# Kernel tuning notes

Measured on AMD Instinct MI355X. Metric: run time of the kernel, lower is better.

Reference implementation:

```python
import jax, jax.numpy as jnp
import numpy as np
from jax.scipy.special import gammaln

D_MODEL = 256
N_HEADS = 8
BIAS_HIDDEN = 64
B, N = 2, 1024
EPS = 1e-4


def setup_inputs() -> dict:
    key = jax.random.key(0)
    ks = jax.random.split(key, 12)
    d, h = D_MODEL, BIAS_HIDDEN
    s = 0.02
    return {
        "src": jax.random.normal(ks[0], (B, N, d), jnp.float32),
        "coords": jax.random.normal(ks[1], (B, N, 4), jnp.float32),
        "Wq": jax.random.normal(ks[2], (d, d), jnp.float32) * s,
        "Wk": jax.random.normal(ks[3], (d, d), jnp.float32) * s,
        "Wv": jax.random.normal(ks[4], (d, d), jnp.float32) * s,
        "Wo": jax.random.normal(ks[5], (d, d), jnp.float32) * s,
        "gw1": jax.random.normal(ks[6], (h, 2), jnp.float32) * s,
        "gb1": jnp.zeros((h,), jnp.float32),
        "gw2": jax.random.normal(ks[7], (1, h), jnp.float32) * s,
        "gb2": jnp.zeros((1,), jnp.float32),
        "dw1": jax.random.normal(ks[8], (h, 4), jnp.float32) * s,
        "db1": jnp.zeros((h,), jnp.float32),
        "dw2": jax.random.normal(ks[9], (2, h), jnp.float32) * s,
        "db2": jnp.zeros((2,), jnp.float32),
    }


def reference(src, coords, Wq, Wk, Wv, Wo, gw1, gb1, gw2, gb2, dw1, db1, dw2, db2):
    Bb, Nn, d = src.shape
    H = N_HEADS
    dh = d // H
    scale = 1.0 / np.sqrt(dh).astype(np.float32)

    def split_heads(x):  # [B,N,d] -> [B,H,N,dh]
        return x.reshape(Bb, Nn, H, dh).transpose(0, 2, 1, 3)

    q = split_heads(src @ Wq.T)
    k = split_heads(src @ Wk.T)
    v = split_heads(src @ Wv.T)

    attn = jnp.einsum("bhnd,bhmd->bhnm", q, k) * scale  # [B,H,N,N]

    xyz = coords[..., :3]
    t = coords[..., 3]
    delta = xyz[:, :, None, :] - xyz[:, None, :, :]        # [B,N,N,3]
    dist = jnp.linalg.norm(delta, axis=-1)                  # [B,N,N]
    dt = t[:, :, None] - t[:, None, :]                      # [B,N,N]

    # geometric bias MLP: 2 -> hidden -> 1
    geom_feat = jnp.stack((dist, dt), axis=-1)              # [B,N,N,2]
    gh = jax.nn.relu(geom_feat @ gw1.T + gb1)
    bias = (gh @ gw2.T + gb2)[..., 0]                       # [B,N,N]

    # delay bias MLP: [dist, xyz_j] (4) -> hidden -> 2 (Gamma shape, rate)
    xyz_j = jnp.broadcast_to(xyz[:, None, :, :], (Bb, Nn, Nn, 3))
    delay_feat = jnp.concatenate((dist[..., None], xyz_j), axis=-1)  # [B,N,N,4]
    dhid = jax.nn.relu(delay_feat @ dw1.T + db1)
    raw = dhid @ dw2.T + db2                                # [B,N,N,2]
    shape = jax.nn.softplus(raw[..., 0]) + EPS
    rate = jax.nn.softplus(raw[..., 1]) + EPS
    dt_pos = jnp.maximum(jnp.abs(dt), EPS)
    # Gamma(shape, rate).log_prob(x)
    log_prob = (shape * jnp.log(rate) + (shape - 1.0) * jnp.log(dt_pos)
                - rate * dt_pos - gammaln(shape))
    bias = bias + log_prob

    attn = attn + bias[:, None, :, :]
    weights = jax.nn.softmax(attn, axis=-1)
    out = jnp.einsum("bhnm,bhmd->bhnd", weights, v)
    out = out.transpose(0, 2, 1, 3).reshape(Bb, Nn, d)
    return out @ Wo.T
```

## Files before the change

kernel.cpp:

```cpp
#include <hip/hip_runtime.h>
#include <hip/hip_bf16.h>
#include <math.h>

constexpr int B_ = 2;
constexpr int N_ = 1024;
constexpr int D_ = 256;
constexpr int H_ = 8;
constexpr int DH_ = 32;
constexpr float SCALE_ = 0.17677669529663687f;
constexpr float LOG2E_ = 1.4426950408889634f;
constexpr float SCALE2_ = SCALE_ * LOG2E_;
constexpr float EPSV_ = 1e-4f;

typedef __attribute__((ext_vector_type(8))) short short8;
typedef __attribute__((ext_vector_type(4))) float f32x4;

__device__ __forceinline__ unsigned short f2bf(float x) {
  __hip_bfloat16 h = __float2bfloat16(x);
  return __builtin_bit_cast(unsigned short, h);
}
__device__ __forceinline__ float bf2f(unsigned short u) {
  unsigned int x = ((unsigned int)u) << 16;
  return __builtin_bit_cast(float, x);
}

__device__ __forceinline__ void split8(const float* __restrict__ p,
                                       short8& hi, short8& lo) {
  f32x4 f0 = *(const f32x4*)p;
  f32x4 f1 = *(const f32x4*)(p + 4);
#pragma unroll
  for (int i = 0; i < 4; ++i) {
    unsigned short h0 = f2bf(f0[i]);
    hi[i] = (short)h0;
    lo[i] = (short)f2bf(f0[i] - bf2f(h0));
    unsigned short h1 = f2bf(f1[i]);
    hi[4 + i] = (short)h1;
    lo[4 + i] = (short)f2bf(f1[i] - bf2f(h1));
  }
}

__device__ __forceinline__ float lgamma_fast(float x) {
  float y = (x < 1.f) ? x : (x - 1.f);
  float g = fmaf(y, 0.035868343f, -0.193527818f);
  g = fmaf(y, g, 0.482199394f);
  g = fmaf(y, g, -0.756704078f);
  g = fmaf(y, g, 0.918206857f);
  g = fmaf(y, g, -0.897056937f);
  g = fmaf(y, g, 0.988205891f);
  g = fmaf(y, g, -0.577191652f);
  g = fmaf(y, g, 1.0f);
  float lg = __logf(g);
  return (x < 1.f) ? lg - __logf(x) : lg;
}
__device__ __forceinline__ float softplus_fast(float x) {
  return __logf(1.f + __expf(x));
}

__device__ __forceinline__
void mfma_proj_wave_f32(const float* __restrict__ A, const float* __restrict__ W,
                        int r0, int c0, f32x4 (&acc)[4]) {
  const int l = threadIdx.x & 63;
  const int lr = l & 15, lg = l >> 4;
#pragma unroll
  for (int ct = 0; ct < 4; ++ct) acc[ct] = (f32x4){0.f, 0.f, 0.f, 0.f};
#pragma unroll 2
  for (int ks = 0; ks < 8; ++ks) {
    short8 ahi, alo;
    split8(A + (size_t)(r0 + lr) * D_ + ks * 32 + lg * 8, ahi, alo);
#pragma unroll
    for (int ct = 0; ct < 4; ++ct) {
      short8 wh, wl;
      split8(W + (size_t)(c0 + ct * 16 + lr) * D_ + ks * 32 + lg * 8, wh, wl);
      acc[ct] = __builtin_amdgcn_mfma_f32_16x16x32_bf16(ahi, wh, acc[ct], 0, 0, 0);
      acc[ct] = __builtin_amdgcn_mfma_f32_16x16x32_bf16(alo, wh, acc[ct], 0, 0, 0);
      acc[ct] = __builtin_amdgcn_mfma_f32_16x16x32_bf16(ahi, wl, acc[ct], 0, 0, 0);
    }
  }
}

__device__ __forceinline__
void mfma_wave_pure(const unsigned short* __restrict__ Ahi,
                    const unsigned short* __restrict__ Alo,
                    const unsigned short* __restrict__ whi,
                    const unsigned short* __restrict__ wlo,
                    int r0, int c0, f32x4 (&acc)[4]) {
  const int l = threadIdx.x & 63;
  const int lr = l & 15, lg = l >> 4;
#pragma unroll
  for (int ct = 0; ct < 4; ++ct) acc[ct] = (f32x4){0.f, 0.f, 0.f, 0.f};
#pragma unroll 2
  for (int ks = 0; ks < 8; ++ks) {
    size_t aoff = (size_t)(r0 + lr) * D_ + ks * 32 + lg * 8;
    short8 ahi = *(const short8*)(Ahi + aoff);
    short8 alo = *(const short8*)(Alo + aoff);
#pragma unroll
    for (int ct = 0; ct < 4; ++ct) {
      size_t woff = (size_t)(c0 + ct * 16 + lr) * D_ + ks * 32 + lg * 8;
      short8 wh = *(const short8*)(whi + woff);
      short8 wl = *(const short8*)(wlo + woff);
      acc[ct] = __builtin_amdgcn_mfma_f32_16x16x32_bf16(ahi, wh, acc[ct], 0, 0, 0);
      acc[ct] = __builtin_amdgcn_mfma_f32_16x16x32_bf16(alo, wh, acc[ct], 0, 0, 0);
      acc[ct] = __builtin_amdgcn_mfma_f32_16x16x32_bf16(ahi, wl, acc[ct], 0, 0, 0);
    }
  }
}

__global__ __launch_bounds__(256)
void fused1_kernel(const float* __restrict__ coords,
                   const float* __restrict__ gw1, const float* __restrict__ gb1,
                   const float* __restrict__ gw2, const float* __restrict__ gb2,
                   const float* __restrict__ dw1, const float* __restrict__ db1,
                   const float* __restrict__ dw2, const float* __restrict__ db2,
                   float* __restrict__ bias,
                   const float* __restrict__ Wq, const float* __restrict__ Wk,
                   const float* __restrict__ Wv, const float* __restrict__ Wo,
                   const float* __restrict__ src,
                   unsigned short* __restrict__ whi, unsigned short* __restrict__ wlo,
                   unsigned short* __restrict__ qbf, unsigned short* __restrict__ kbf,
                   unsigned short* __restrict__ vtbf) {
  const int tid = threadIdx.x;
  const int bi = blockIdx.x;

  if (bi >= 2432) {
    int idx = ((bi - 2432) * 256 + tid) * 4;
    float4 f = *(const float4*)(Wo + idx);
    ushort4 hi, lo;
    hi.x = f2bf(f.x); lo.x = f2bf(f.x - bf2f(hi.x));
    hi.y = f2bf(f.y); lo.y = f2bf(f.y - bf2f(hi.y));
    hi.z = f2bf(f.z); lo.z = f2bf(f.z - bf2f(hi.z));
    hi.w = f2bf(f.w); lo.w = f2bf(f.w - bf2f(hi.w));
    *(ushort4*)(whi + 3 * 65536 + idx) = hi;
    *(ushort4*)(wlo + 3 * 65536 + idx) = lo;
    return;
  }

  if (bi >= 2048) {
    const int bi2 = bi - 2048;
    const int z = bi2 >> 7;
    const float* W = (z == 0) ? Wq : (z == 1) ? Wk : Wv;
    const int rem = bi2 & 127;
    const int by = rem >> 5, bx = rem & 31;
    const int w = tid >> 6;
    const int r0 = bx * 64 + w * 16;
    const int c0 = by * 64;
    f32x4 acc[4];
    mfma_proj_wave_f32(src, W, r0, c0, acc);

    const int l = tid & 63, lr = l & 15, lg = l >> 4;
    if (z < 2) {
      unsigned short* dst = (z == 0) ? qbf : kbf;
#pragma unroll
      for (int ct = 0; ct < 4; ++ct) {
        int o = c0 + ct * 16 + lr, h = o >> 5, d = o & 31;
#pragma unroll
        for (int r = 0; r < 4; ++r) {
          int R = r0 + lg * 4 + r, b = R >> 10, n = R & 1023;
          dst[(size_t)((b * H_ + h) * N_ + n) * DH_ + d] = f2bf(acc[ct][r]);
        }
      }
    } else {
#pragma unroll
      for (int ct = 0; ct < 4; ++ct) {
        int o = c0 + ct * 16 + lr, h = o >> 5, d = o & 31;
#pragma unroll
        for (int r = 0; r < 4; ++r) {
          int R = r0 + lg * 4 + r, b = R >> 10, n = R & 1023;
          vtbf[(size_t)((b * H_ + h) * DH_ + d) * N_ + n] = f2bf(acc[ct][r]);
        }
      }
    }
    return;
  }

  const int jt = bi & 3;
  const int it = (bi >> 2) & 255;
  const int b  = bi >> 10;
  const int j  = jt * 256 + tid;
  const int ibase = it * 4;

  const float4 cj = ((const float4*)coords)[b * N_ + j];

  float dist[4], dtv[4];
#pragma unroll
  for (int ii = 0; ii < 4; ++ii) {
    const float* cp = coords + 4 * (b * N_ + ibase + ii);
    float dx = cp[0] - cj.x, dy = cp[1] - cj.y, dz = cp[2] - cj.z;
    dist[ii] = sqrtf(dx * dx + dy * dy + dz * dz);
    dtv[ii]  = cp[3] - cj.w;
  }

  const float db20 = db2[0], db21 = db2[1], gb20 = gb2[0];
  float biasv[4], raw0[4], raw1[4];
#pragma unroll
  for (int ii = 0; ii < 4; ++ii) { biasv[ii] = 0.f; raw0[ii] = db20; raw1[ii] = db21; }

#pragma unroll 4
  for (int h = 0; h < 64; ++h) {
    float g0 = gw1[2 * h], g1 = gw1[2 * h + 1], gb = gb1[h], g2 = gw2[h];
    float w0 = dw1[4 * h], wx = dw1[4 * h + 1], wy = dw1[4 * h + 2], wz = dw1[4 * h + 3];
    float c0 = db1[h], c1 = dw2[h], c2 = dw2[64 + h];
    float dp = fmaf(wx, cj.x, fmaf(wy, cj.y, fmaf(wz, cj.z, c0)));
#pragma unroll
    for (int ii = 0; ii < 4; ++ii) {
      float g = fmaf(g0, dist[ii], fmaf(g1, dtv[ii], gb));
      biasv[ii] = fmaf(g2, fmaxf(g, 0.f), biasv[ii]);
      float dh_ = fmaxf(fmaf(w0, dist[ii], dp), 0.f);
      raw0[ii] = fmaf(c1, dh_, raw0[ii]);
      raw1[ii] = fmaf(c2, dh_, raw1[ii]);
    }
  }

#pragma unroll
  for (int ii = 0; ii < 4; ++ii) {
    float sh  = softplus_fast(raw0[ii]) + EPSV_;
    float ra  = softplus_fast(raw1[ii]) + EPSV_;
    float dtp = fmaxf(fabsf(dtv[ii]), EPSV_);
    float lp  = sh * __logf(ra) + (sh - 1.f) * __logf(dtp) - ra * dtp - lgamma_fast(sh);
    bias[(size_t)(b * N_ + ibase + ii) * N_ + j] = (biasv[ii] + gb20 + lp) * LOG2E_;
  }
}

__global__ __launch_bounds__(512)
void attn_kernel(const unsigned short* __restrict__ qbf,
                 const unsigned short* __restrict__ kbf,
                 const unsigned short* __restrict__ vtbf,
                 const float* __restrict__ biasg,
                 unsigned short* __restrict__ ophi,
                 unsigned short* __restrict__ oplo) {
  __shared__ __align__(16) unsigned short p_lds[8][16][72];
  __shared__ float acc_lds[3][2][16][32];
  __shared__ float ml_lds[3][2][16][2];

  const int tid = threadIdx.x;
  const int w = tid >> 6, l = tid & 63;
  const int s = w >> 2, jq = w & 3;
  const int lr = l & 15, lg = l >> 4;
  const int bh = blockIdx.x >> 5;
  const int qb = blockIdx.x & 31;
  const int b = bh >> 3, h = bh & 7;
  const int ibase = qb * 32 + s * 16;

  const short8 ones8 = {16256, 16256, 16256, 16256, 16256, 16256, 16256, 16256};

  const short8 qfrag =
      *(const short8*)(qbf + (size_t)(bh * N_ + ibase + lr) * DH_ + lg * 8);
  const unsigned short* kb = kbf + (size_t)bh * N_ * DH_;
  const unsigned short* vb = vtbf + (size_t)bh * DH_ * N_;
  const float* bbase = biasg + (size_t)b * N_ * N_;

  f32x4 acc[2], accL;
  acc[0] = (f32x4){0.f, 0.f, 0.f, 0.f};
  acc[1] = (f32x4){0.f, 0.f, 0.f, 0.f};
  accL   = (f32x4){0.f, 0.f, 0.f, 0.f};
  float m_run[4];
#pragma unroll
  for (int r = 0; r < 4; ++r) m_run[r] = -3e38f;

  const int jbeg = jq * 256;
  for (int j0 = jbeg; j0 < jbeg + 256; j0 += 64) {
    f32x4 sc[4];
#pragma unroll
    for (int t = 0; t < 4; ++t) {
      short8 kf = *(const short8*)(kb + (size_t)(j0 + t * 16 + lr) * DH_ + lg * 8);
      sc[t] = __builtin_amdgcn_mfma_f32_16x16x32_bf16(
          qfrag, kf, (f32x4){0.f, 0.f, 0.f, 0.f}, 0, 0, 0);
    }
#pragma unroll
    for (int r = 0; r < 4; ++r) {
      const float* bi = bbase + (size_t)(ibase + lg * 4 + r) * N_ + j0 + lr;
#pragma unroll
      for (int t = 0; t < 4; ++t)
        sc[t][r] = fmaf(sc[t][r], SCALE2_, bi[t * 16]);
    }
    float mt[4];
#pragma unroll
    for (int r = 0; r < 4; ++r)
      mt[r] = fmaxf(fmaxf(sc[0][r], sc[1][r]), fmaxf(sc[2][r], sc[3][r]));
#pragma unroll
    for (int off = 1; off < 16; off <<= 1)
#pragma unroll
      for (int r = 0; r < 4; ++r)
        mt[r] = fmaxf(mt[r], __shfl_xor(mt[r], off));
    float corr[4];
#pragma unroll
    for (int r = 0; r < 4; ++r) {
      float mn = fmaxf(m_run[r], mt[r]);
      corr[r] = exp2f(m_run[r] - mn);
      m_run[r] = mn;
    }
#pragma unroll
    for (int t = 0; t < 4; ++t)
#pragma unroll
      for (int r = 0; r < 4; ++r)
        sc[t][r] = exp2f(sc[t][r] - m_run[r]);
#pragma unroll
    for (int r = 0; r < 4; ++r) {
      acc[0][r] *= corr[r];
      acc[1][r] *= corr[r];
      accL[r]   *= corr[r];
    }
#pragma unroll
    for (int t = 0; t < 4; ++t)
#pragma unroll
      for (int r = 0; r < 4; ++r)
        p_lds[w][lg * 4 + r][t * 16 + lr] = f2bf(sc[t][r]);
#pragma unroll
    for (int kc = 0; kc < 2; ++kc) {
      short8 pf = *(const short8*)&p_lds[w][lr][kc * 32 + lg * 8];
#pragma unroll
      for (int c = 0; c < 2; ++c) {
        short8 vf = *(const short8*)(vb + (size_t)(c * 16 + lr) * N_ +
                                     j0 + kc * 32 + lg * 8);
        acc[c] = __builtin_amdgcn_mfma_f32_16x16x32_bf16(pf, vf, acc[c], 0, 0, 0);
      }
      accL = __builtin_amdgcn_mfma_f32_16x16x32_bf16(pf, ones8, accL, 0, 0, 0);
    }
  }

  if (jq > 0) {
#pragma unroll
    for (int c = 0; c < 2; ++c)
#pragma unroll
      for (int r = 0; r < 4; ++r)
        acc_lds[jq - 1][s][lg * 4 + r][c * 16 + lr] = acc[c][r];
    if (lr == 0) {
#pragma unroll
      for (int r = 0; r < 4; ++r) {
        ml_lds[jq - 1][s][lg * 4 + r][0] = m_run[r];
        ml_lds[jq - 1][s][lg * 4 + r][1] = accL[r];
      }
    }
  }
  __syncthreads();
  if (jq == 0) {
    float c0[4], cq[3][4], linv[4];
#pragma unroll
    for (int r = 0; r < 4; ++r) {
      int row = lg * 4 + r;
      float m = m_run[r];
#pragma unroll
      for (int q = 0; q < 3; ++q) m = fmaxf(m, ml_lds[q][s][row][0]);
      c0[r] = exp2f(m_run[r] - m);
      float lsum = accL[r] * c0[r];
#pragma unroll
      for (int q = 0; q < 3; ++q) {
        cq[q][r] = exp2f(ml_lds[q][s][row][0] - m);
        lsum = fmaf(ml_lds[q][s][row][1], cq[q][r], lsum);
      }
      linv[r] = 1.f / lsum;
    }
#pragma unroll
    for (int c = 0; c < 2; ++c) {
#pragma unroll
      for (int r = 0; r < 4; ++r) {
        int row = lg * 4 + r;
        int i = ibase + row;
        int d = c * 16 + lr;
        float o = acc[c][r] * c0[r];
#pragma unroll
        for (int q = 0; q < 3; ++q)
          o = fmaf(acc_lds[q][s][row][d], cq[q][r], o);
        o *= linv[r];
        size_t oidx = (size_t)(b * N_ + i) * D_ + h * DH_ + d;
        unsigned short hi = f2bf(o);
        ophi[oidx] = hi;
        oplo[oidx] = f2bf(o - bf2f(hi));
      }
    }
  }
}

__global__ __launch_bounds__(256)
void projo_kernel(const unsigned short* __restrict__ ophi,
                  const unsigned short* __restrict__ oplo,
                  const unsigned short* __restrict__ whi,
                  const unsigned short* __restrict__ wlo,
                  float* __restrict__ out) {
  const int w = threadIdx.x >> 6;
  const int r0 = blockIdx.x * 64 + w * 16;
  const int c0 = blockIdx.y * 64;
  f32x4 acc[4];
  mfma_wave_pure(ophi, oplo, whi + 3 * 65536, wlo + 3 * 65536, r0, c0, acc);
  const int l = threadIdx.x & 63, lr = l & 15, lg = l >> 4;
#pragma unroll
  for (int ct = 0; ct < 4; ++ct)
#pragma unroll
    for (int r = 0; r < 4; ++r)
      out[(size_t)(r0 + lg * 4 + r) * D_ + c0 + ct * 16 + lr] = acc[ct][r];
}

extern "C" void kernel_launch(void* const* d_in, const int* in_sizes, int n_in,
                              void* d_out, int out_size, void* d_ws, size_t ws_size,
                              hipStream_t stream) {
  const float* src    = (const float*)d_in[0];
  const float* coords = (const float*)d_in[1];
  const float* Wq  = (const float*)d_in[2];
  const float* Wk  = (const float*)d_in[3];
  const float* Wv  = (const float*)d_in[4];
  const float* Wo  = (const float*)d_in[5];
  const float* gw1 = (const float*)d_in[6];
  const float* gb1 = (const float*)d_in[7];
  const float* gw2 = (const float*)d_in[8];
  const float* gb2 = (const float*)d_in[9];
  const float* dw1 = (const float*)d_in[10];
  const float* db1 = (const float*)d_in[11];
  const float* dw2 = (const float*)d_in[12];
  const float* db2 = (const float*)d_in[13];
  float* out = (float*)d_out;

  char* wsb = (char*)d_ws;
  unsigned short* qbf  = (unsigned short*)wsb;
  unsigned short* kbf  = (unsigned short*)(wsb + (1 << 20));
  unsigned short* vtbf = (unsigned short*)(wsb + (2 << 20));
  float* biasw         = (float*)(wsb + (3 << 20));
  unsigned short* whi  = (unsigned short*)(wsb + (11 << 20));
  unsigned short* wlo  = (unsigned short*)(wsb + (11 << 20) + (512 << 10));
  unsigned short* ophi = (unsigned short*)(wsb + (14 << 20));
  unsigned short* oplo = (unsigned short*)(wsb + (15 << 20));

  fused1_kernel<<<2496, 256, 0, stream>>>(coords, gw1, gb1, gw2, gb2,
                                          dw1, db1, dw2, db2, biasw,
                                          Wq, Wk, Wv, Wo, src,
                                          whi, wlo, qbf, kbf, vtbf);
  attn_kernel<<<512, 512, 0, stream>>>(qbf, kbf, vtbf, biasw, ophi, oplo);
  projo_kernel<<<dim3(32, 4), 256, 0, stream>>>(ophi, oplo, whi, wlo, out);
}
```

Baseline: 79.61 us.

## Fuse attention and output projection via software grid barrier

Merges the attention kernel and the output-projection kernel into one launch. An atomic-counter grid barrier separates the two phases, and the first 64 blocks then run the Wo projection. This removes one kernel launch and its inter-kernel gap. In exchange it adds a memset launch and an atomic spin barrier. The barrier relies on all 512 blocks being co-resident, which is not guaranteed, so the kernel risks deadlock.

```diff
diff --git a/kernel.cpp b/kernel.cpp
--- a/kernel.cpp
+++ b/kernel.cpp
@@ -11,6 +11,7 @@
 constexpr float LOG2E_ = 1.4426950408889634f;
 constexpr float SCALE2_ = SCALE_ * LOG2E_;
 constexpr float EPSV_ = 1e-4f;
+constexpr unsigned GRID2_ = 512;
 
 typedef __attribute__((ext_vector_type(8))) short short8;
 typedef __attribute__((ext_vector_type(4))) float f32x4;
@@ -56,10 +57,25 @@
   return __logf(1.f + __expf(x));
 }
 
+__device__ __forceinline__ void grid_barrier(unsigned* bar) {
+  __syncthreads();
+  if (threadIdx.x == 0) {
+    __threadfence();
+    unsigned old = atomicAdd(bar, 1u);
+    if (old == GRID2_ - 1) {
+      atomicExch(bar + 1, 1u);
+    } else {
+      while (atomicAdd(bar + 1, 0u) == 0u)
+        __builtin_amdgcn_s_sleep(2);
+    }
+    __threadfence();
+  }
+  __syncthreads();
+}
+
 __device__ __forceinline__
 void mfma_proj_wave_f32(const float* __restrict__ A, const float* __restrict__ W,
-                        int r0, int c0, f32x4 (&acc)[4]) {
-  const int l = threadIdx.x & 63;
+                        int r0, int c0, int l, f32x4 (&acc)[4]) {
   const int lr = l & 15, lg = l >> 4;
 #pragma unroll
   for (int ct = 0; ct < 4; ++ct) acc[ct] = (f32x4){0.f, 0.f, 0.f, 0.f};
@@ -83,8 +99,7 @@
                     const unsigned short* __restrict__ Alo,
                     const unsigned short* __restrict__ whi,
                     const unsigned short* __restrict__ wlo,
-                    int r0, int c0, f32x4 (&acc)[4]) {
-  const int l = threadIdx.x & 63;
+                    int r0, int c0, int l, f32x4 (&acc)[4]) {
   const int lr = l & 15, lg = l >> 4;
 #pragma unroll
   for (int ct = 0; ct < 4; ++ct) acc[ct] = (f32x4){0.f, 0.f, 0.f, 0.f};
@@ -144,7 +159,7 @@
     const int r0 = bx * 64 + w * 16;
     const int c0 = by * 64;
     f32x4 acc[4];
-    mfma_proj_wave_f32(src, W, r0, c0, acc);
+    mfma_proj_wave_f32(src, W, r0, c0, tid & 63, acc);
 
     const int l = tid & 63, lr = l & 15, lg = l >> 4;
     if (z < 2) {
@@ -220,173 +235,180 @@
   }
 }
 
-__global__ __launch_bounds__(512)
-void attn_kernel(const unsigned short* __restrict__ qbf,
-                 const unsigned short* __restrict__ kbf,
-                 const unsigned short* __restrict__ vtbf,
-                 const float* __restrict__ biasg,
-                 unsigned short* __restrict__ ophi,
-                 unsigned short* __restrict__ oplo) {
+__global__ __launch_bounds__(512, 4)
+void attn_projo_kernel(const unsigned short* __restrict__ qbf,
+                       const unsigned short* __restrict__ kbf,
+                       const unsigned short* __restrict__ vtbf,
+                       const float* __restrict__ biasg,
+                       const unsigned short* __restrict__ whi,
+                       const unsigned short* __restrict__ wlo,
+                       unsigned short* __restrict__ ophi,
+                       unsigned short* __restrict__ oplo,
+                       float* __restrict__ out,
+                       unsigned* __restrict__ bar) {
   __shared__ __align__(16) unsigned short p_lds[8][16][72];
   __shared__ float acc_lds[3][2][16][32];
   __shared__ float ml_lds[3][2][16][2];
 
   const int tid = threadIdx.x;
-  const int w = tid >> 6, l = tid & 63;
-  const int s = w >> 2, jq = w & 3;
-  const int lr = l & 15, lg = l >> 4;
-  const int bh = blockIdx.x >> 5;
-  const int qb = blockIdx.x & 31;
-  const int b = bh >> 3, h = bh & 7;
-  const int ibase = qb * 32 + s * 16;
-
-  const short8 ones8 = {16256, 16256, 16256, 16256, 16256, 16256, 16256, 16256};
-
-  const short8 qfrag =
-      *(const short8*)(qbf + (size_t)(bh * N_ + ibase + lr) * DH_ + lg * 8);
-  const unsigned short* kb = kbf + (size_t)bh * N_ * DH_;
-  const unsigned short* vb = vtbf + (size_t)bh * DH_ * N_;
-  const float* bbase = biasg + (size_t)b * N_ * N_;
-
-  f32x4 acc[2], accL;
-  acc[0] = (f32x4){0.f, 0.f, 0.f, 0.f};
-  acc[1] = (f32x4){0.f, 0.f, 0.f, 0.f};
-  accL   = (f32x4){0.f, 0.f, 0.f, 0.f};
-  float m_run[4];
-#pragma unroll
-  for (int r = 0; r < 4; ++r) m_run[r] = -3e38f;
-
-  const int jbeg = jq * 256;
-  for (int j0 = jbeg; j0 < jbeg + 256; j0 += 64) {
-    f32x4 sc[4];
-#pragma unroll
-    for (int t = 0; t < 4; ++t) {
-      short8 kf = *(const short8*)(kb + (size_t)(j0 + t * 16 + lr) * DH_ + lg * 8);
-      sc[t] = __builtin_amdgcn_mfma_f32_16x16x32_bf16(
-          qfrag, kf, (f32x4){0.f, 0.f, 0.f, 0.f}, 0, 0, 0);
-    }
-#pragma unroll
-    for (int r = 0; r < 4; ++r) {
-      const float* bi = bbase + (size_t)(ibase + lg * 4 + r) * N_ + j0 + lr;
+  const int bi = blockIdx.x;
+
+  {
+    const int w = tid >> 6, l = tid & 63;
+    const int s = w >> 2, jq = w & 3;
+    const int lr = l & 15, lg = l >> 4;
+    const int bh = bi >> 5;
+    const int qb = bi & 31;
+    const int b = bh >> 3, h = bh & 7;
+    const int ibase = qb * 32 + s * 16;
+
+    const short8 ones8 = {16256, 16256, 16256, 16256, 16256, 16256, 16256, 16256};
+    const short8 qfrag =
+        *(const short8*)(qbf + (size_t)(bh * N_ + ibase + lr) * DH_ + lg * 8);
+    const unsigned short* kb = kbf + (size_t)bh * N_ * DH_;
+    const unsigned short* vb = vtbf + (size_t)bh * DH_ * N_;
+    const float* bbase = biasg + (size_t)b * N_ * N_;
+
+    f32x4 acc[2], accL;
+    acc[0] = (f32x4){0.f, 0.f, 0.f, 0.f};
+    acc[1] = (f32x4){0.f, 0.f, 0.f, 0.f};
+    accL   = (f32x4){0.f, 0.f, 0.f, 0.f};
+    float m_run[4];
+#pragma unroll
+    for (int r = 0; r < 4; ++r) m_run[r] = -3e38f;
+
+    const int jbeg = jq * 256;
+    for (int j0 = jbeg; j0 < jbeg + 256; j0 += 64) {
+      f32x4 sc[4];
+#pragma unroll
+      for (int t = 0; t < 4; ++t) {
+        short8 kf = *(const short8*)(kb + (size_t)(j0 + t * 16 + lr) * DH_ + lg * 8);
+        sc[t] = __builtin_amdgcn_mfma_f32_16x16x32_bf16(
+            qfrag, kf, (f32x4){0.f, 0.f, 0.f, 0.f}, 0, 0, 0);
+      }
+#pragma unroll
+      for (int r = 0; r < 4; ++r) {
+        const float* bp = bbase + (size_t)(ibase + lg * 4 + r) * N_ + j0 + lr;
+#pragma unroll
+        for (int t = 0; t < 4; ++t)
+          sc[t][r] = fmaf(sc[t][r], SCALE2_, bp[t * 16]);
+      }
+      float mt[4];
+#pragma unroll
+      for (int r = 0; r < 4; ++r)
+        mt[r] = fmaxf(fmaxf(sc[0][r], sc[1][r]), fmaxf(sc[2][r], sc[3][r]));
+#pragma unroll
+      for (int off = 1; off < 16; off <<= 1)
+#pragma unroll
+        for (int r = 0; r < 4; ++r)
+          mt[r] = fmaxf(mt[r], __shfl_xor(mt[r], off));
+      float corr[4];
+#pragma unroll
+      for (int r = 0; r < 4; ++r) {
+        float mn = fmaxf(m_run[r], mt[r]);
+        corr[r] = exp2f(m_run[r] - mn);
+        m_run[r] = mn;
+      }
 #pragma unroll
       for (int t = 0; t < 4; ++t)
-        sc[t][r] = fmaf(sc[t][r], SCALE2_, bi[t * 16]);
-    }
-    float mt[4];
-#pragma unroll
-    for (int r = 0; r < 4; ++r)
-      mt[r] = fmaxf(fmaxf(sc[0][r], sc[1][r]), fmaxf(sc[2][r], sc[3][r]));
-#pragma unroll
-    for (int off = 1; off < 16; off <<= 1)
-#pragma unroll
-      for (int r = 0; r < 4; ++r)
-        mt[r] = fmaxf(mt[r], __shfl_xor(mt[r], off));
-    float corr[4];
-#pragma unroll
-    for (int r = 0; r < 4; ++r) {
-      float mn = fmaxf(m_run[r], mt[r]);
-      corr[r] = exp2f(m_run[r] - mn);
-      m_run[r] = mn;
-    }
-#pragma unroll
-    for (int t = 0; t < 4; ++t)
-#pragma unroll
-      for (int r = 0; r < 4; ++r)
-        sc[t][r] = exp2f(sc[t][r] - m_run[r]);
-#pragma unroll
-    for (int r = 0; r < 4; ++r) {
-      acc[0][r] *= corr[r];
-      acc[1][r] *= corr[r];
-      accL[r]   *= corr[r];
-    }
-#pragma unroll
-    for (int t = 0; t < 4; ++t)
-#pragma unroll
-      for (int r = 0; r < 4; ++r)
-        p_lds[w][lg * 4 + r][t * 16 + lr] = f2bf(sc[t][r]);
-#pragma unroll
-    for (int kc = 0; kc < 2; ++kc) {
-      short8 pf = *(const short8*)&p_lds[w][lr][kc * 32 + lg * 8];
-#pragma unroll
-      for (int c = 0; c < 2; ++c) {
-        short8 vf = *(const short8*)(vb + (size_t)(c * 16 + lr) * N_ +
-                                     j0 + kc * 32 + lg * 8);
-        acc[c] = __builtin_amdgcn_mfma_f32_16x16x32_bf16(pf, vf, acc[c], 0, 0, 0);
-      }
-      accL = __builtin_amdgcn_mfma_f32_16x16x32_bf16(pf, ones8, accL, 0, 0, 0);
-    }
-  }
-
-  if (jq > 0) {
-#pragma unroll
-    for (int c = 0; c < 2; ++c)
-#pragma unroll
-      for (int r = 0; r < 4; ++r)
-        acc_lds[jq - 1][s][lg * 4 + r][c * 16 + lr] = acc[c][r];
-    if (lr == 0) {
+#pragma unroll
+        for (int r = 0; r < 4; ++r)
+          sc[t][r] = exp2f(sc[t][r] - m_run[r]);
 #pragma unroll
       for (int r = 0; r < 4; ++r) {
-        ml_lds[jq - 1][s][lg * 4 + r][0] = m_run[r];
-        ml_lds[jq - 1][s][lg * 4 + r][1] = accL[r];
-      }
-    }
-  }
-  __syncthreads();
-  if (jq == 0) {
-    float c0[4], cq[3][4], linv[4];
-#pragma unroll
-    for (int r = 0; r < 4; ++r) {
-      int row = lg * 4 + r;
-      float m = m_run[r];
-#pragma unroll
-      for (int q = 0; q < 3; ++q) m = fmaxf(m, ml_lds[q][s][row][0]);
-      c0[r] = exp2f(m_run[r] - m);
-      float lsum = accL[r] * c0[r];
-#pragma unroll
-      for (int q = 0; q < 3; ++q) {
-        cq[q][r] = exp2f(ml_lds[q][s][row][0] - m);
-        lsum = fmaf(ml_lds[q][s][row][1], cq[q][r], lsum);
-      }
-      linv[r] = 1.f / lsum;
-    }
-#pragma unroll
-    for (int c = 0; c < 2; ++c) {
+        acc[0][r] *= corr[r];
+        acc[1][r] *= corr[r];
+        accL[r]   *= corr[r];
+      }
+#pragma unroll
+      for (int t = 0; t < 4; ++t)
+#pragma unroll
+        for (int r = 0; r < 4; ++r)
+          p_lds[w][lg * 4 + r][t * 16 + lr] = f2bf(sc[t][r]);
+#pragma unroll
+      for (int kc = 0; kc < 2; ++kc) {
+        short8 pf = *(const short8*)&p_lds[w][lr][kc * 32 + lg * 8];
+#pragma unroll
+        for (int c = 0; c < 2; ++c) {
+          short8 vf = *(const short8*)(vb + (size_t)(c * 16 + lr) * N_ +
+                                       j0 + kc * 32 + lg * 8);
+          acc[c] = __builtin_amdgcn_mfma_f32_16x16x32_bf16(pf, vf, acc[c], 0, 0, 0);
+        }
+        accL = __builtin_amdgcn_mfma_f32_16x16x32_bf16(pf, ones8, accL, 0, 0, 0);
+      }
+    }
+
+    if (jq > 0) {
+#pragma unroll
+      for (int c = 0; c < 2; ++c)
+#pragma unroll
+        for (int r = 0; r < 4; ++r)
+          acc_lds[jq - 1][s][lg * 4 + r][c * 16 + lr] = acc[c][r];
+      if (lr == 0) {
+#pragma unroll
+        for (int r = 0; r < 4; ++r) {
+          ml_lds[jq - 1][s][lg * 4 + r][0] = m_run[r];
+          ml_lds[jq - 1][s][lg * 4 + r][1] = accL[r];
+        }
+      }
+    }
+    __syncthreads();
+    if (jq == 0) {
+      float c0[4], cq[3][4], linv[4];
 #pragma unroll
       for (int r = 0; r < 4; ++r) {
         int row = lg * 4 + r;
-        int i = ibase + row;
-        int d = c * 16 + lr;
-        float o = acc[c][r] * c0[r];
-#pragma unroll
-        for (int q = 0; q < 3; ++q)
-          o = fmaf(acc_lds[q][s][row][d], cq[q][r], o);
-        o *= linv[r];
-        size_t oidx = (size_t)(b * N_ + i) * D_ + h * DH_ + d;
-        unsigned short hi = f2bf(o);
-        ophi[oidx] = hi;
-        oplo[oidx] = f2bf(o - bf2f(hi));
-      }
-    }
-  }
-}
-
-__global__ __launch_bounds__(256)
-void projo_kernel(const unsigned short* __restrict__ ophi,
-                  const unsigned short* __restrict__ oplo,
-                  const unsigned short* __restrict__ whi,
-                  const unsigned short* __restrict__ wlo,
-                  float* __restrict__ out) {
-  const int w = threadIdx.x >> 6;
-  const int r0 = blockIdx.x * 64 + w * 16;
-  const int c0 = blockIdx.y * 64;
-  f32x4 acc[4];
-  mfma_wave_pure(ophi, oplo, whi + 3 * 65536, wlo + 3 * 65536, r0, c0, acc);
-  const int l = threadIdx.x & 63, lr = l & 15, lg = l >> 4;
-#pragma unroll
-  for (int ct = 0; ct < 4; ++ct)
-#pragma unroll
-    for (int r = 0; r < 4; ++r)
-      out[(size_t)(r0 + lg * 4 + r) * D_ + c0 + ct * 16 + lr] = acc[ct][r];
+        float m = m_run[r];
+#pragma unroll
+        for (int q = 0; q < 3; ++q) m = fmaxf(m, ml_lds[q][s][row][0]);
+        c0[r] = exp2f(m_run[r] - m);
+        float lsum = accL[r] * c0[r];
+#pragma unroll
+        for (int q = 0; q < 3; ++q) {
+          cq[q][r] = exp2f(ml_lds[q][s][row][0] - m);
+          lsum = fmaf(ml_lds[q][s][row][1], cq[q][r], lsum);
+        }
+        linv[r] = 1.f / lsum;
+      }
+#pragma unroll
+      for (int c = 0; c < 2; ++c) {
+#pragma unroll
+        for (int r = 0; r < 4; ++r) {
+          int row = lg * 4 + r;
+          int i = ibase + row;
+          int d = c * 16 + lr;
+          float o = acc[c][r] * c0[r];
+#pragma unroll
+          for (int q = 0; q < 3; ++q)
+            o = fmaf(acc_lds[q][s][row][d], cq[q][r], o);
+          o *= linv[r];
+          size_t oidx = (size_t)(b * N_ + i) * D_ + h * DH_ + d;
+          unsigned short hi = f2bf(o);
+          ophi[oidx] = hi;
+          oplo[oidx] = f2bf(o - bf2f(hi));
+        }
+      }
+    }
+  }
+
+  grid_barrier(bar);
+
+  if (bi < 64) {
+    const int u = bi * 2 + (tid >> 8);
+    const int utid = tid & 255;
+    const int by = u >> 5, bx = u & 31;
+    const int w = utid >> 6, l = utid & 63;
+    const int r0 = bx * 64 + w * 16;
+    const int c0 = by * 64;
+    f32x4 acc[4];
+    mfma_wave_pure(ophi, oplo, whi + 3 * 65536, wlo + 3 * 65536, r0, c0, l, acc);
+    const int lr = l & 15, lg = l >> 4;
+#pragma unroll
+    for (int ct = 0; ct < 4; ++ct)
+#pragma unroll
+      for (int r = 0; r < 4; ++r)
+        out[(size_t)(r0 + lg * 4 + r) * D_ + c0 + ct * 16 + lr] = acc[ct][r];
+  }
 }
 
 extern "C" void kernel_launch(void* const* d_in, const int* in_sizes, int n_in,
@@ -417,11 +439,13 @@
   unsigned short* wlo  = (unsigned short*)(wsb + (11 << 20) + (512 << 10));
   unsigned short* ophi = (unsigned short*)(wsb + (14 << 20));
   unsigned short* oplo = (unsigned short*)(wsb + (15 << 20));
-
+  unsigned* bar        = (unsigned*)(wsb + (16 << 20));
+
+  hipMemsetAsync(bar, 0, 64, stream);
   fused1_kernel<<<2496, 256, 0, stream>>>(coords, gw1, gb1, gw2, gb2,
                                           dw1, db1, dw2, db2, biasw,
                                           Wq, Wk, Wv, Wo, src,
                                           whi, wlo, qbf, kbf, vtbf);
-  attn_kernel<<<512, 512, 0, stream>>>(qbf, kbf, vtbf, biasw, ophi, oplo);
-  projo_kernel<<<dim3(32, 4), 256, 0, stream>>>(ophi, oplo, whi, wlo, out);
-}
+  attn_projo_kernel<<<GRID2_, 512, 0, stream>>>(qbf, kbf, vtbf, biasw,
+                                                whi, wlo, ophi, oplo, out, bar);
+}
```

Measured after the change: 143.9 us. 80.7% more time.
